# Optimization experiments

Measured on AMD Instinct MI355X. Metric: run time of the kernel, lower is better.

Reference implementation:

```python
import jax, jax.numpy as jnp
import numpy as np

TOP_K = 2
SMOOTHING = 0.9


def setup_inputs() -> dict:
    key = jax.random.key(0)
    k1, k2, k3 = jax.random.split(key, 3)
    T, D, E = 16384, 2048, 64
    x = jax.random.normal(k1, (T, D), dtype=jnp.float32)
    gate_w = jax.random.normal(k2, (D, E), dtype=jnp.float32) * (1.0 / np.sqrt(D))
    expert_loads = jax.random.uniform(k3, (E,), dtype=jnp.float32)
    expert_loads = expert_loads / jnp.sum(expert_loads)  # normalized load estimate
    return {"x": x, "gate_w": gate_w, "expert_loads": expert_loads}


def reference(x, gate_w, expert_loads):
    T, _ = x.shape
    E = gate_w.shape[1]
    # Gate projection: [T, D] @ [D, E] -> [T, E]
    logits = jnp.matmul(x, gate_w)
    # Load-balancing bias injection (ExpertLoadBalancer.get_balancing_biases):
    # bias = -(load - 1/E) * 2, added to logits for expert *selection* only.
    biases = -(expert_loads - 1.0 / E) * 2.0
    _, top_idx = jax.lax.top_k(logits + biases[None, :], TOP_K)  # [T, K] int32
    # Routing weights: softmax over the selected (unbiased) logits.
    top_logits = jnp.take_along_axis(logits, top_idx, axis=1)  # [T, K]
    routing_weights = jax.nn.softmax(top_logits, axis=-1)  # [T, K]
    # Vectorized load update (replaces the Python double loop in update_loads):
    # scatter-add routing weights per expert, normalize by token count, EMA-smooth.
    current_loads = jax.ops.segment_sum(
        routing_weights.reshape(-1), top_idx.reshape(-1), num_segments=E
    ) / T
    new_loads = SMOOTHING * expert_loads + (1.0 - SMOOTHING) * current_loads
    return routing_weights, top_idx, new_loads
```

## Files before the change

kernel.cpp:

```cpp
#include <hip/hip_runtime.h>

#define TT 16384
#define DD 2048
#define EE 64

typedef __attribute__((ext_vector_type(8))) short bf16x8;
typedef __attribute__((ext_vector_type(8))) unsigned short ushort8;
typedef __attribute__((ext_vector_type(4))) float f32x4;

__device__ __forceinline__ unsigned short bf16_rne(float f) {
    unsigned u = __float_as_uint(f);
    return (unsigned short)((u + 0x7FFFu + ((u >> 16) & 1u)) >> 16);
}
__device__ __forceinline__ float bf16_f32(unsigned short h) {
    return __uint_as_float(((unsigned)h) << 16);
}
__device__ __forceinline__ unsigned cvt_pk(float lo, float hi) {
    unsigned r;
    asm("v_cvt_pk_bf16_f32 %0, %1, %2" : "=v"(r) : "v"(lo), "v"(hi));
    return r;
}
__device__ __forceinline__ bf16x8 pack4(unsigned a, unsigned b, unsigned c, unsigned d) {
    union { unsigned u[4]; bf16x8 v; } t;
    t.u[0] = a; t.u[1] = b; t.u[2] = c; t.u[3] = d;
    return t.v;
}
__device__ __forceinline__ void gload16(void* lds, const void* g) {
    __builtin_amdgcn_global_load_lds(
        (const __attribute__((address_space(1))) unsigned int*)g,
        (__attribute__((address_space(3))) unsigned int*)lds, 16, 0, 0);
}

__global__ __launch_bounds__(256)
void wconv(const float* __restrict__ wg, unsigned short* __restrict__ wpack) {
    const int t = (int)blockIdx.x * 256 + threadIdx.x;
    const int K0 = t >> 9, h = (t >> 8) & 1, m = (t >> 6) & 3, lane = t & 63;
    const int e = m * 16 + (lane & 15);
    const int ks = K0 * 32 + (lane >> 4) * 8;
    ushort8 v;
#pragma unroll
    for (int j = 0; j < 8; ++j) {
        const float f = wg[(size_t)(ks + j) * EE + e];
        const unsigned short hi = bf16_rne(f);
        v[j] = h ? bf16_rne(f - bf16_f32(hi)) : hi;
    }
    *(ushort8*)(wpack + ((size_t)(K0 * 8 + h * 4 + m) * 64 + lane) * 8) = v;
}

__global__ __launch_bounds__(512, 4)
void gate_fused(const float* __restrict__ x, const unsigned short* __restrict__ wpack,
                const float* __restrict__ loads, float* __restrict__ out,
                float* __restrict__ binpart) {
    __shared__ __align__(16) float arena[12288];
    __shared__ float bins[2][64];

    const int tid = threadIdx.x, lane = tid & 63, w = tid >> 6;
    const int tg = w >> 2, q = w & 3;
    const int tb = (int)blockIdx.x;

    f32x4 acc[4] = {{0,0,0,0},{0,0,0,0},{0,0,0,0},{0,0,0,0}};

    auto stage_x = [&](int s, float* rb) {
#pragma unroll
        for (int i = 0; i < 2; ++i) {
            const int rowp = lane >> 3;
            const int r = i * 8 + rowp;
            const int c = (lane & 7) ^ rowp;
            gload16(rb + i * 256,
                    x + (size_t)(tb * 32 + tg * 16 + r) * DD + q * 512 + s * 32 + c * 4);
        }
    };
    auto loadW = [&](int t, bf16x8 (&wh)[4], bf16x8 (&wl)[4]) {
        const unsigned short* base = wpack + (size_t)(q * 16 + t) * 4096 + lane * 8;
#pragma unroll
        for (int m = 0; m < 4; ++m) {
            wh[m] = *(const bf16x8*)(base + (size_t)m * 512);
            wl[m] = *(const bf16x8*)(base + (size_t)(4 + m) * 512);
        }
    };
    auto compute = [&](const float* rb, bf16x8 (&wh)[4], bf16x8 (&wl)[4]) {
        const int r = lane & 15;
        const int kgc = (lane >> 4) << 1;
        const int sw = r & 7;
        const f32x4 va = *(const f32x4*)(rb + r * 32 + ((kgc) ^ sw) * 4);
        const f32x4 vb = *(const f32x4*)(rb + r * 32 + ((kgc + 1) ^ sw) * 4);
        const float cf[8] = {va.x, va.y, va.z, va.w, vb.x, vb.y, vb.z, vb.w};
        unsigned ph[4], pl[4];
#pragma unroll
        for (int j = 0; j < 4; ++j) {
            ph[j] = cvt_pk(cf[2 * j], cf[2 * j + 1]);
            const float h0 = __uint_as_float(ph[j] << 16);
            const float h1 = __uint_as_float(ph[j] & 0xFFFF0000u);
            pl[j] = cvt_pk(cf[2 * j] - h0, cf[2 * j + 1] - h1);
        }
        const bf16x8 bhi = pack4(ph[0], ph[1], ph[2], ph[3]);
        const bf16x8 blo = pack4(pl[0], pl[1], pl[2], pl[3]);
#pragma unroll
        for (int m = 0; m < 4; ++m) {
            acc[m] = __builtin_amdgcn_mfma_f32_16x16x32_bf16(wh[m], bhi, acc[m], 0, 0, 0);
            acc[m] = __builtin_amdgcn_mfma_f32_16x16x32_bf16(wh[m], blo, acc[m], 0, 0, 0);
            acc[m] = __builtin_amdgcn_mfma_f32_16x16x32_bf16(wl[m], bhi, acc[m], 0, 0, 0);
        }
    };

    float* ring = arena + (size_t)w * 1536;
    float *p0 = ring, *p1 = ring + 512, *p2 = ring + 1024;
    bf16x8 whA[4], wlA[4], whB[4], wlB[4];

    stage_x(0, p0);
    stage_x(1, p1);
    loadW(0, whA, wlA);
    asm volatile("s_waitcnt vmcnt(10)" ::: "memory");

#pragma unroll 1
    for (int s = 0; s < 14; s += 2) {
        stage_x(s + 2, p2);
        loadW(s + 1, whB, wlB);
        compute(p0, whA, wlA);
        asm volatile("s_waitcnt vmcnt(10)" ::: "memory");
        { float* t_ = p0; p0 = p1; p1 = p2; p2 = t_; }

        stage_x(s + 3, p2);
        loadW(s + 2, whA, wlA);
        compute(p0, whB, wlB);
        asm volatile("s_waitcnt vmcnt(10)" ::: "memory");
        { float* t_ = p0; p0 = p1; p1 = p2; p2 = t_; }
    }
    loadW(15, whB, wlB);
    compute(p0, whA, wlA);
    asm volatile("s_waitcnt vmcnt(8)" ::: "memory");
    compute(p1, whB, wlB);

    __syncthreads();
    float* accb = arena;
    if (q != 0) {
#pragma unroll
        for (int m = 0; m < 4; ++m)
            *(f32x4*)(accb + ((size_t)((q - 1) * 128 + tg * 64 + lane) * 20 + m * 4)) = acc[m];
    }
    __syncthreads();
    if (q != 0) return;

    f32x4 r[4];
#pragma unroll
    for (int m = 0; m < 4; ++m) {
        f32x4 s_ = acc[m];
#pragma unroll
        for (int qq = 0; qq < 3; ++qq) {
            const f32x4 t_ =
                *(const f32x4*)(accb + ((size_t)(qq * 128 + tg * 64 + lane) * 20 + m * 4));
            s_.x += t_.x; s_.y += t_.y; s_.z += t_.z; s_.w += t_.w;
        }
        r[m] = s_;
    }

    const int col = lane & 15;
    const int tok = tb * 32 + tg * 16 + col;
    const int erow = (lane >> 4) * 4;
    float v1 = -3.4e38f, u1 = 0.0f, v2 = -3.4e38f, u2 = 0.0f;
    int i1 = 0x7fffffff, i2 = 0x7fffffff;
#pragma unroll
    for (int m = 0; m < 4; ++m)
#pragma unroll
        for (int rr = 0; rr < 4; ++rr) {
            const int e = m * 16 + erow + rr;
            const float u = r[m][rr];
            const float b = u - (loads[e] - 0.015625f) * 2.0f;
            if ((b > v1) || (b == v1 && e < i1)) {
                v2 = v1; u2 = u1; i2 = i1;
                v1 = b;  u1 = u;  i1 = e;
            } else if ((b > v2) || (b == v2 && e < i2)) {
                v2 = b; u2 = u; i2 = e;
            }
        }
#pragma unroll
    for (int s = 0; s < 2; ++s) {
        const int mask = 16 << s;
        const float ov1 = __shfl_xor(v1, mask), ou1 = __shfl_xor(u1, mask);
        const float ov2 = __shfl_xor(v2, mask), ou2 = __shfl_xor(u2, mask);
        const int oi1 = __shfl_xor(i1, mask), oi2 = __shfl_xor(i2, mask);
        if ((ov1 > v1) || (ov1 == v1 && oi1 < i1)) {
            if ((v1 > ov2) || (v1 == ov2 && i1 < oi2)) { v2 = v1; u2 = u1; i2 = i1; }
            else                                        { v2 = ov2; u2 = ou2; i2 = oi2; }
            v1 = ov1; u1 = ou1; i1 = oi1;
        } else if ((ov1 > v2) || (ov1 == v2 && oi1 < i2)) {
            v2 = ov1; u2 = ou1; i2 = oi1;
        }
    }

    bins[tg][lane] = 0.0f;
    if (lane < 16) {
        const float mx = fmaxf(u1, u2);
        const float e1 = __expf(u1 - mx), e2 = __expf(u2 - mx);
        const float w1 = e1 / (e1 + e2), w2 = e2 / (e1 + e2);
        *(float2*)(out + 2 * tok) = make_float2(w1, w2);
        *(float2*)(out + 2 * TT + 2 * tok) = make_float2((float)i1, (float)i2);
        atomicAdd(&bins[tg][i1], w1);
        atomicAdd(&bins[tg][i2], w2);
    }
    binpart[(size_t)(tb * 2 + tg) * 64 + lane] = bins[tg][lane];
}

__global__ __launch_bounds__(1024)
void finalize(const float* __restrict__ binpart, const float* __restrict__ loads,
              float* __restrict__ out) {
    __shared__ float p[16][64];
    const int e = threadIdx.x & 63, sub = threadIdx.x >> 6;
    float s = 0.0f;
#pragma unroll
    for (int r = 0; r < 64; ++r)
        s += binpart[(size_t)(sub * 64 + r) * 64 + e];
    p[sub][e] = s;
    __syncthreads();
    if (sub == 0) {
        float tot = 0.0f;
#pragma unroll
        for (int k = 0; k < 16; ++k) tot += p[k][e];
        out[4 * TT + e] = 0.9f * loads[e] + 0.1f * (tot * (1.0f / 16384.0f));
    }
}

extern "C" void kernel_launch(void* const* d_in, const int* in_sizes, int n_in,
                              void* d_out, int out_size, void* d_ws, size_t ws_size,
                              hipStream_t stream) {
    const float* x = (const float*)d_in[0];
    const float* wg = (const float*)d_in[1];
    const float* loads = (const float*)d_in[2];
    float* out = (float*)d_out;

    unsigned short* wpack = (unsigned short*)d_ws;
    float* binpart = (float*)(wpack + (size_t)64 * 8 * 64 * 8);

    hipLaunchKernelGGL(wconv, dim3(128), dim3(256), 0, stream, wg, wpack);
    hipLaunchKernelGGL(gate_fused, dim3(512), dim3(512), 0, stream,
                       x, wpack, loads, out, binpart);
    hipLaunchKernelGGL(finalize, dim3(1), dim3(1024), 0, stream,
                       binpart, loads, out);
}
```

Measured before the change: 46.27 us.

## Halve gate block to 16 tokens and deepen weight prefetch with asm loads

Each gate block now has four waves covering 16 tokens instead of eight waves covering 32, and twice as many blocks are launched. Weight fragments are loaded through inline-asm global loads fenced by scheduling barriers, and are now prefetched one stage further ahead alongside the x tiles, with explicit vmcnt waits. The aim is better overlap of the x stream and weight loads with MFMA work, plus finer-grained scheduling. The cost is that every block still reads the whole packed weight matrix, so total L2 weight traffic doubles. The inline asm also takes control of instruction ordering away from the compiler.

After: 45.17 us. -2.4%, faster.

```diff
diff --git a/kernel.cpp b/kernel.cpp
--- a/kernel.cpp
+++ b/kernel.cpp
@@ -30,6 +30,11 @@
         (const __attribute__((address_space(1))) unsigned int*)g,
         (__attribute__((address_space(3))) unsigned int*)lds, 16, 0, 0);
 }
+__device__ __forceinline__ void ld16(bf16x8& d, const void* p) {
+    asm volatile("global_load_dwordx4 %0, %1, off"
+                 : "=&v"(d) : "v"(p) : "memory");
+}
+#define SB0() __builtin_amdgcn_sched_barrier(0)
 
 __global__ __launch_bounds__(256)
 void wconv(const float* __restrict__ wg, unsigned short* __restrict__ wpack) {
@@ -47,15 +52,14 @@
     *(ushort8*)(wpack + ((size_t)(K0 * 8 + h * 4 + m) * 64 + lane) * 8) = v;
 }
 
-__global__ __launch_bounds__(512, 4)
+__global__ __launch_bounds__(256, 4)
 void gate_fused(const float* __restrict__ x, const unsigned short* __restrict__ wpack,
                 const float* __restrict__ loads, float* __restrict__ out,
                 float* __restrict__ binpart) {
-    __shared__ __align__(16) float arena[12288];
-    __shared__ float bins[2][64];
-
-    const int tid = threadIdx.x, lane = tid & 63, w = tid >> 6;
-    const int tg = w >> 2, q = w & 3;
+    __shared__ __align__(16) float arena[6144];
+    __shared__ float bins[64];
+
+    const int tid = threadIdx.x, lane = tid & 63, q = tid >> 6;
     const int tb = (int)blockIdx.x;
 
     f32x4 acc[4] = {{0,0,0,0},{0,0,0,0},{0,0,0,0},{0,0,0,0}};
@@ -67,16 +71,15 @@
             const int r = i * 8 + rowp;
             const int c = (lane & 7) ^ rowp;
             gload16(rb + i * 256,
-                    x + (size_t)(tb * 32 + tg * 16 + r) * DD + q * 512 + s * 32 + c * 4);
+                    x + (size_t)(tb * 16 + r) * DD + q * 512 + s * 32 + c * 4);
         }
     };
-    auto loadW = [&](int t, bf16x8 (&wh)[4], bf16x8 (&wl)[4]) {
+    auto asmW = [&](int t, bf16x8 (&wh)[4], bf16x8 (&wl)[4]) {
         const unsigned short* base = wpack + (size_t)(q * 16 + t) * 4096 + lane * 8;
 #pragma unroll
-        for (int m = 0; m < 4; ++m) {
-            wh[m] = *(const bf16x8*)(base + (size_t)m * 512);
-            wl[m] = *(const bf16x8*)(base + (size_t)(4 + m) * 512);
-        }
+        for (int m = 0; m < 4; ++m) ld16(wh[m], base + (size_t)m * 512);
+#pragma unroll
+        for (int m = 0; m < 4; ++m) ld16(wl[m], base + (size_t)(4 + m) * 512);
     };
     auto compute = [&](const float* rb, bf16x8 (&wh)[4], bf16x8 (&wl)[4]) {
         const int r = lane & 15;
@@ -103,40 +106,58 @@
         }
     };
 
-    float* ring = arena + (size_t)w * 1536;
+    float* ring = arena + (size_t)q * 1536;
     float *p0 = ring, *p1 = ring + 512, *p2 = ring + 1024;
     bf16x8 whA[4], wlA[4], whB[4], wlB[4];
 
-    stage_x(0, p0);
-    stage_x(1, p1);
-    loadW(0, whA, wlA);
+    stage_x(0, p0); SB0();
+    asmW(0, whA, wlA); SB0();
+    stage_x(1, p1); SB0();
+    asmW(1, whB, wlB); SB0();
+    stage_x(2, p2); SB0();
+    asm volatile("s_waitcnt vmcnt(12)" ::: "memory");
+    SB0();
+    compute(p0, whA, wlA);
+    { float* t_ = p0; p0 = p1; p1 = p2; p2 = t_; }
+
+#pragma unroll 1
+    for (int s = 0; s < 12; s += 2) {
+        asmW(s + 2, whA, wlA); SB0();
+        stage_x(s + 3, p2); SB0();
+        asm volatile("s_waitcnt vmcnt(12)" ::: "memory");
+        SB0();
+        compute(p0, whB, wlB);
+        { float* t_ = p0; p0 = p1; p1 = p2; p2 = t_; }
+
+        asmW(s + 3, whB, wlB); SB0();
+        stage_x(s + 4, p2); SB0();
+        asm volatile("s_waitcnt vmcnt(12)" ::: "memory");
+        SB0();
+        compute(p0, whA, wlA);
+        { float* t_ = p0; p0 = p1; p1 = p2; p2 = t_; }
+    }
+    asmW(14, whA, wlA); SB0();
+    stage_x(15, p2); SB0();
+    asm volatile("s_waitcnt vmcnt(12)" ::: "memory");
+    SB0();
+    compute(p0, whB, wlB);
+    { float* t_ = p0; p0 = p1; p1 = p2; p2 = t_; }
+
+    asmW(15, whB, wlB); SB0();
     asm volatile("s_waitcnt vmcnt(10)" ::: "memory");
-
-#pragma unroll 1
-    for (int s = 0; s < 14; s += 2) {
-        stage_x(s + 2, p2);
-        loadW(s + 1, whB, wlB);
-        compute(p0, whA, wlA);
-        asm volatile("s_waitcnt vmcnt(10)" ::: "memory");
-        { float* t_ = p0; p0 = p1; p1 = p2; p2 = t_; }
-
-        stage_x(s + 3, p2);
-        loadW(s + 2, whA, wlA);
-        compute(p0, whB, wlB);
-        asm volatile("s_waitcnt vmcnt(10)" ::: "memory");
-        { float* t_ = p0; p0 = p1; p1 = p2; p2 = t_; }
-    }
-    loadW(15, whB, wlB);
+    SB0();
     compute(p0, whA, wlA);
-    asm volatile("s_waitcnt vmcnt(8)" ::: "memory");
-    compute(p1, whB, wlB);
+    { float* t_ = p0; p0 = p1; p1 = p2; p2 = t_; }
+    asm volatile("s_waitcnt vmcnt(0)" ::: "memory");
+    SB0();
+    compute(p0, whB, wlB);
 
     __syncthreads();
     float* accb = arena;
     if (q != 0) {
 #pragma unroll
         for (int m = 0; m < 4; ++m)
-            *(f32x4*)(accb + ((size_t)((q - 1) * 128 + tg * 64 + lane) * 20 + m * 4)) = acc[m];
+            *(f32x4*)(accb + ((size_t)((q - 1) * 64 + lane) * 20 + m * 4)) = acc[m];
     }
     __syncthreads();
     if (q != 0) return;
@@ -148,14 +169,14 @@
 #pragma unroll
         for (int qq = 0; qq < 3; ++qq) {
             const f32x4 t_ =
-                *(const f32x4*)(accb + ((size_t)(qq * 128 + tg * 64 + lane) * 20 + m * 4));
+                *(const f32x4*)(accb + ((size_t)(qq * 64 + lane) * 20 + m * 4));
             s_.x += t_.x; s_.y += t_.y; s_.z += t_.z; s_.w += t_.w;
         }
         r[m] = s_;
     }
 
     const int col = lane & 15;
-    const int tok = tb * 32 + tg * 16 + col;
+    const int tok = tb * 16 + col;
     const int erow = (lane >> 4) * 4;
     float v1 = -3.4e38f, u1 = 0.0f, v2 = -3.4e38f, u2 = 0.0f;
     int i1 = 0x7fffffff, i2 = 0x7fffffff;
@@ -188,17 +209,17 @@
         }
     }
 
-    bins[tg][lane] = 0.0f;
+    bins[lane] = 0.0f;
     if (lane < 16) {
         const float mx = fmaxf(u1, u2);
         const float e1 = __expf(u1 - mx), e2 = __expf(u2 - mx);
         const float w1 = e1 / (e1 + e2), w2 = e2 / (e1 + e2);
         *(float2*)(out + 2 * tok) = make_float2(w1, w2);
         *(float2*)(out + 2 * TT + 2 * tok) = make_float2((float)i1, (float)i2);
-        atomicAdd(&bins[tg][i1], w1);
-        atomicAdd(&bins[tg][i2], w2);
-    }
-    binpart[(size_t)(tb * 2 + tg) * 64 + lane] = bins[tg][lane];
+        atomicAdd(&bins[i1], w1);
+        atomicAdd(&bins[i2], w2);
+    }
+    binpart[(size_t)tb * 64 + lane] = bins[lane];
 }
 
 __global__ __launch_bounds__(1024)
@@ -232,7 +253,7 @@
     float* binpart = (float*)(wpack + (size_t)64 * 8 * 64 * 8);
 
     hipLaunchKernelGGL(wconv, dim3(128), dim3(256), 0, stream, wg, wpack);
-    hipLaunchKernelGGL(gate_fused, dim3(512), dim3(512), 0, stream,
+    hipLaunchKernelGGL(gate_fused, dim3(1024), dim3(256), 0, stream,
                        x, wpack, loads, out, binpart);
     hipLaunchKernelGGL(finalize, dim3(1), dim3(1024), 0, stream,
                        binpart, loads, out);
```

## Let each wave compute 32 tokens so weight fragments are reused twice

Applied to the files above, without the earlier changes.

The block shrinks from 512 to 256 threads. Each wave now handles 32 tokens using two accumulator sets, so each weight fragment loaded from global memory feeds two token tiles and weight traffic per token is halved. The K loop is fully unrolled into a three-stage ring for both x and W, with explicit waitcnt and sched_barrier placement, and top-k runs twice per wave. The cost is higher register pressure from triple-buffered weights and doubled accumulators, and fewer waves per block, which may reduce latency hiding.

Result: faster. 40.19 us (median of 3 runs) (-13.1%).

```diff
diff --git a/kernel.cpp b/kernel.cpp
--- a/kernel.cpp
+++ b/kernel.cpp
@@ -30,6 +30,7 @@
         (const __attribute__((address_space(1))) unsigned int*)g,
         (__attribute__((address_space(3))) unsigned int*)lds, 16, 0, 0);
 }
+#define SB0() __builtin_amdgcn_sched_barrier(0)
 
 __global__ __launch_bounds__(256)
 void wconv(const float* __restrict__ wg, unsigned short* __restrict__ wpack) {
@@ -47,43 +48,50 @@
     *(ushort8*)(wpack + ((size_t)(K0 * 8 + h * 4 + m) * 64 + lane) * 8) = v;
 }
 
-__global__ __launch_bounds__(512, 4)
+__global__ __launch_bounds__(256, 2)
 void gate_fused(const float* __restrict__ x, const unsigned short* __restrict__ wpack,
                 const float* __restrict__ loads, float* __restrict__ out,
                 float* __restrict__ binpart) {
     __shared__ __align__(16) float arena[12288];
-    __shared__ float bins[2][64];
-
-    const int tid = threadIdx.x, lane = tid & 63, w = tid >> 6;
-    const int tg = w >> 2, q = w & 3;
+    __shared__ float bins[64];
+
+    const int tid = threadIdx.x, lane = tid & 63, q = tid >> 6;
     const int tb = (int)blockIdx.x;
 
-    f32x4 acc[4] = {{0,0,0,0},{0,0,0,0},{0,0,0,0},{0,0,0,0}};
-
-    auto stage_x = [&](int s, float* rb) {
-#pragma unroll
-        for (int i = 0; i < 2; ++i) {
+    f32x4 a0[4] = {{0,0,0,0},{0,0,0,0},{0,0,0,0},{0,0,0,0}};
+    f32x4 a1[4] = {{0,0,0,0},{0,0,0,0},{0,0,0,0},{0,0,0,0}};
+
+    float* ring = arena + (size_t)q * 3072;
+    float *sp0 = ring, *sp1 = ring + 1024, *sp2 = ring + 2048;
+
+    auto stage_x = [&](int s, float* sb) {
+#pragma unroll
+        for (int i = 0; i < 4; ++i) {
             const int rowp = lane >> 3;
-            const int r = i * 8 + rowp;
             const int c = (lane & 7) ^ rowp;
-            gload16(rb + i * 256,
-                    x + (size_t)(tb * 32 + tg * 16 + r) * DD + q * 512 + s * 32 + c * 4);
-        }
-    };
-    auto loadW = [&](int t, bf16x8 (&wh)[4], bf16x8 (&wl)[4]) {
-        const unsigned short* base = wpack + (size_t)(q * 16 + t) * 4096 + lane * 8;
+            gload16(sb + i * 256,
+                    x + (size_t)(tb * 32 + i * 8 + rowp) * DD + q * 512 + s * 32 + c * 4);
+        }
+    };
+    auto loadW = [&](int s, bf16x8 (&wh)[4], bf16x8 (&wl)[4]) {
+        const unsigned short* base = wpack + (size_t)(q * 16 + s) * 4096 + lane * 8;
 #pragma unroll
         for (int m = 0; m < 4; ++m) {
             wh[m] = *(const bf16x8*)(base + (size_t)m * 512);
             wl[m] = *(const bf16x8*)(base + (size_t)(4 + m) * 512);
         }
     };
-    auto compute = [&](const float* rb, bf16x8 (&wh)[4], bf16x8 (&wl)[4]) {
-        const int r = lane & 15;
+    auto readx = [&](const float* sb, f32x4& va0, f32x4& vb0, f32x4& va1, f32x4& vb1) {
+        const int rl = lane & 15;
         const int kgc = (lane >> 4) << 1;
-        const int sw = r & 7;
-        const f32x4 va = *(const f32x4*)(rb + r * 32 + ((kgc) ^ sw) * 4);
-        const f32x4 vb = *(const f32x4*)(rb + r * 32 + ((kgc + 1) ^ sw) * 4);
+        const int sw = rl & 7;
+        va0 = *(const f32x4*)(sb + rl * 32 + ((kgc) ^ sw) * 4);
+        vb0 = *(const f32x4*)(sb + rl * 32 + ((kgc + 1) ^ sw) * 4);
+        va1 = *(const f32x4*)(sb + (16 + rl) * 32 + ((kgc) ^ sw) * 4);
+        vb1 = *(const f32x4*)(sb + (16 + rl) * 32 + ((kgc + 1) ^ sw) * 4);
+    };
+    auto domfma = [&](const f32x4& va, const f32x4& vb,
+                      bf16x8 (&wh)[4], bf16x8 (&wl)[4], f32x4 (&ac)[4]) {
         const float cf[8] = {va.x, va.y, va.z, va.w, vb.x, vb.y, vb.z, vb.w};
         unsigned ph[4], pl[4];
 #pragma unroll
@@ -97,108 +105,119 @@
         const bf16x8 blo = pack4(pl[0], pl[1], pl[2], pl[3]);
 #pragma unroll
         for (int m = 0; m < 4; ++m) {
-            acc[m] = __builtin_amdgcn_mfma_f32_16x16x32_bf16(wh[m], bhi, acc[m], 0, 0, 0);
-            acc[m] = __builtin_amdgcn_mfma_f32_16x16x32_bf16(wh[m], blo, acc[m], 0, 0, 0);
-            acc[m] = __builtin_amdgcn_mfma_f32_16x16x32_bf16(wl[m], bhi, acc[m], 0, 0, 0);
-        }
-    };
-
-    float* ring = arena + (size_t)w * 1536;
-    float *p0 = ring, *p1 = ring + 512, *p2 = ring + 1024;
-    bf16x8 whA[4], wlA[4], whB[4], wlB[4];
-
-    stage_x(0, p0);
-    stage_x(1, p1);
-    loadW(0, whA, wlA);
-    asm volatile("s_waitcnt vmcnt(10)" ::: "memory");
-
-#pragma unroll 1
-    for (int s = 0; s < 14; s += 2) {
-        stage_x(s + 2, p2);
-        loadW(s + 1, whB, wlB);
-        compute(p0, whA, wlA);
-        asm volatile("s_waitcnt vmcnt(10)" ::: "memory");
-        { float* t_ = p0; p0 = p1; p1 = p2; p2 = t_; }
-
-        stage_x(s + 3, p2);
-        loadW(s + 2, whA, wlA);
-        compute(p0, whB, wlB);
-        asm volatile("s_waitcnt vmcnt(10)" ::: "memory");
-        { float* t_ = p0; p0 = p1; p1 = p2; p2 = t_; }
-    }
-    loadW(15, whB, wlB);
-    compute(p0, whA, wlA);
-    asm volatile("s_waitcnt vmcnt(8)" ::: "memory");
-    compute(p1, whB, wlB);
+            ac[m] = __builtin_amdgcn_mfma_f32_16x16x32_bf16(wh[m], bhi, ac[m], 0, 0, 0);
+            ac[m] = __builtin_amdgcn_mfma_f32_16x16x32_bf16(wh[m], blo, ac[m], 0, 0, 0);
+            ac[m] = __builtin_amdgcn_mfma_f32_16x16x32_bf16(wl[m], bhi, ac[m], 0, 0, 0);
+        }
+    };
+
+    bf16x8 WH0[4], WO0[4], WH1[4], WO1[4], WH2[4], WO2[4];
+
+    stage_x(0, sp0); SB0();
+    loadW(0, WH0, WO0); SB0();
+    stage_x(1, sp1); SB0();
+    loadW(1, WH1, WO1); SB0();
+    stage_x(2, sp2); SB0();
+
+#define ITER(s, nsl, nwl, VM, DOW, DOS)                                   \
+    do {                                                                  \
+        asm volatile("s_waitcnt vmcnt(" #VM ")" ::: "memory"); SB0();     \
+        f32x4 va0, vb0, va1, vb1;                                         \
+        readx(sp##nsl, va0, vb0, va1, vb1); SB0();                        \
+        asm volatile("s_waitcnt lgkmcnt(0)" ::: "memory"); SB0();         \
+        if (DOW) loadW((s) + 2, WH##nwl, WO##nwl);                        \
+        SB0();                                                            \
+        if (DOS) stage_x((s) + 3, sp##nsl);                               \
+        SB0();                                                            \
+        domfma(va0, vb0, WH##nsl, WO##nsl, a0);                           \
+        domfma(va1, vb1, WH##nsl, WO##nsl, a1);                           \
+    } while (0)
+
+    ITER(0, 0, 2, 16, 1, 1);  ITER(1, 1, 0, 16, 1, 1);
+    ITER(2, 2, 1, 16, 1, 1);  ITER(3, 0, 2, 16, 1, 1);
+    ITER(4, 1, 0, 16, 1, 1);  ITER(5, 2, 1, 16, 1, 1);
+    ITER(6, 0, 2, 16, 1, 1);  ITER(7, 1, 0, 16, 1, 1);
+    ITER(8, 2, 1, 16, 1, 1);  ITER(9, 0, 2, 16, 1, 1);
+    ITER(10, 1, 0, 16, 1, 1); ITER(11, 2, 1, 16, 1, 1);
+    ITER(12, 0, 2, 16, 1, 1);
+    ITER(13, 1, 0, 16, 1, 0);
+    ITER(14, 2, 0, 12, 0, 0);
+    ITER(15, 0, 0, 0, 0, 0);
+#undef ITER
 
     __syncthreads();
-    float* accb = arena;
     if (q != 0) {
-#pragma unroll
-        for (int m = 0; m < 4; ++m)
-            *(f32x4*)(accb + ((size_t)((q - 1) * 128 + tg * 64 + lane) * 20 + m * 4)) = acc[m];
+        float* p = arena + (size_t)(q - 1) * 2304 + lane * 36;
+#pragma unroll
+        for (int m = 0; m < 4; ++m) {
+            *(f32x4*)(p + m * 4) = a0[m];
+            *(f32x4*)(p + 16 + m * 4) = a1[m];
+        }
     }
     __syncthreads();
     if (q != 0) return;
 
-    f32x4 r[4];
-#pragma unroll
-    for (int m = 0; m < 4; ++m) {
-        f32x4 s_ = acc[m];
-#pragma unroll
-        for (int qq = 0; qq < 3; ++qq) {
-            const f32x4 t_ =
-                *(const f32x4*)(accb + ((size_t)(qq * 128 + tg * 64 + lane) * 20 + m * 4));
-            s_.x += t_.x; s_.y += t_.y; s_.z += t_.z; s_.w += t_.w;
-        }
-        r[m] = s_;
-    }
-
+#pragma unroll 1
+    for (int qq = 0; qq < 3; ++qq) {
+        const float* p = arena + (size_t)qq * 2304 + lane * 36;
+#pragma unroll
+        for (int m = 0; m < 4; ++m) {
+            const f32x4 t0 = *(const f32x4*)(p + m * 4);
+            const f32x4 t1 = *(const f32x4*)(p + 16 + m * 4);
+            a0[m].x += t0.x; a0[m].y += t0.y; a0[m].z += t0.z; a0[m].w += t0.w;
+            a1[m].x += t1.x; a1[m].y += t1.y; a1[m].z += t1.z; a1[m].w += t1.w;
+        }
+    }
+
+    bins[lane] = 0.0f;
     const int col = lane & 15;
-    const int tok = tb * 32 + tg * 16 + col;
     const int erow = (lane >> 4) * 4;
-    float v1 = -3.4e38f, u1 = 0.0f, v2 = -3.4e38f, u2 = 0.0f;
-    int i1 = 0x7fffffff, i2 = 0x7fffffff;
-#pragma unroll
-    for (int m = 0; m < 4; ++m)
-#pragma unroll
-        for (int rr = 0; rr < 4; ++rr) {
-            const int e = m * 16 + erow + rr;
-            const float u = r[m][rr];
-            const float b = u - (loads[e] - 0.015625f) * 2.0f;
-            if ((b > v1) || (b == v1 && e < i1)) {
-                v2 = v1; u2 = u1; i2 = i1;
-                v1 = b;  u1 = u;  i1 = e;
-            } else if ((b > v2) || (b == v2 && e < i2)) {
-                v2 = b; u2 = u; i2 = e;
+    auto topk = [&](f32x4 (&r)[4], int tokbase) {
+        float v1 = -3.4e38f, u1 = 0.0f, v2 = -3.4e38f, u2 = 0.0f;
+        int i1 = 0x7fffffff, i2 = 0x7fffffff;
+#pragma unroll
+        for (int m = 0; m < 4; ++m)
+#pragma unroll
+            for (int rr = 0; rr < 4; ++rr) {
+                const int e = m * 16 + erow + rr;
+                const float u = r[m][rr];
+                const float b = u - (loads[e] - 0.015625f) * 2.0f;
+                if ((b > v1) || (b == v1 && e < i1)) {
+                    v2 = v1; u2 = u1; i2 = i1;
+                    v1 = b;  u1 = u;  i1 = e;
+                } else if ((b > v2) || (b == v2 && e < i2)) {
+                    v2 = b; u2 = u; i2 = e;
+                }
             }
-        }
-#pragma unroll
-    for (int s = 0; s < 2; ++s) {
-        const int mask = 16 << s;
-        const float ov1 = __shfl_xor(v1, mask), ou1 = __shfl_xor(u1, mask);
-        const float ov2 = __shfl_xor(v2, mask), ou2 = __shfl_xor(u2, mask);
-        const int oi1 = __shfl_xor(i1, mask), oi2 = __shfl_xor(i2, mask);
-        if ((ov1 > v1) || (ov1 == v1 && oi1 < i1)) {
-            if ((v1 > ov2) || (v1 == ov2 && i1 < oi2)) { v2 = v1; u2 = u1; i2 = i1; }
-            else                                        { v2 = ov2; u2 = ou2; i2 = oi2; }
-            v1 = ov1; u1 = ou1; i1 = oi1;
-        } else if ((ov1 > v2) || (ov1 == v2 && oi1 < i2)) {
-            v2 = ov1; u2 = ou1; i2 = oi1;
-        }
-    }
-
-    bins[tg][lane] = 0.0f;
-    if (lane < 16) {
-        const float mx = fmaxf(u1, u2);
-        const float e1 = __expf(u1 - mx), e2 = __expf(u2 - mx);
-        const float w1 = e1 / (e1 + e2), w2 = e2 / (e1 + e2);
-        *(float2*)(out + 2 * tok) = make_float2(w1, w2);
-        *(float2*)(out + 2 * TT + 2 * tok) = make_float2((float)i1, (float)i2);
-        atomicAdd(&bins[tg][i1], w1);
-        atomicAdd(&bins[tg][i2], w2);
-    }
-    binpart[(size_t)(tb * 2 + tg) * 64 + lane] = bins[tg][lane];
+#pragma unroll
+        for (int s = 0; s < 2; ++s) {
+            const int mask = 16 << s;
+            const float ov1 = __shfl_xor(v1, mask), ou1 = __shfl_xor(u1, mask);
+            const float ov2 = __shfl_xor(v2, mask), ou2 = __shfl_xor(u2, mask);
+            const int oi1 = __shfl_xor(i1, mask), oi2 = __shfl_xor(i2, mask);
+            if ((ov1 > v1) || (ov1 == v1 && oi1 < i1)) {
+                if ((v1 > ov2) || (v1 == ov2 && i1 < oi2)) { v2 = v1; u2 = u1; i2 = i1; }
+                else                                        { v2 = ov2; u2 = ou2; i2 = oi2; }
+                v1 = ov1; u1 = ou1; i1 = oi1;
+            } else if ((ov1 > v2) || (ov1 == v2 && oi1 < i2)) {
+                v2 = ov1; u2 = ou1; i2 = oi1;
+            }
+        }
+        if (lane < 16) {
+            const int tok = tokbase + col;
+            const float mx = fmaxf(u1, u2);
+            const float e1 = __expf(u1 - mx), e2 = __expf(u2 - mx);
+            const float w1 = e1 / (e1 + e2), w2 = e2 / (e1 + e2);
+            *(float2*)(out + 2 * tok) = make_float2(w1, w2);
+            *(float2*)(out + 2 * TT + 2 * tok) = make_float2((float)i1, (float)i2);
+            atomicAdd(&bins[i1], w1);
+            atomicAdd(&bins[i2], w2);
+        }
+    };
+    topk(a0, tb * 32);
+    topk(a1, tb * 32 + 16);
+
+    binpart[(size_t)tb * 64 + lane] = bins[lane];
 }
 
 __global__ __launch_bounds__(1024)
@@ -208,8 +227,8 @@
     const int e = threadIdx.x & 63, sub = threadIdx.x >> 6;
     float s = 0.0f;
 #pragma unroll
-    for (int r = 0; r < 64; ++r)
-        s += binpart[(size_t)(sub * 64 + r) * 64 + e];
+    for (int r = 0; r < 32; ++r)
+        s += binpart[(size_t)(sub * 32 + r) * 64 + e];
     p[sub][e] = s;
     __syncthreads();
     if (sub == 0) {
@@ -232,7 +251,7 @@
     float* binpart = (float*)(wpack + (size_t)64 * 8 * 64 * 8);
 
     hipLaunchKernelGGL(wconv, dim3(128), dim3(256), 0, stream, wg, wpack);
-    hipLaunchKernelGGL(gate_fused, dim3(512), dim3(512), 0, stream,
+    hipLaunchKernelGGL(gate_fused, dim3(512), dim3(256), 0, stream,
                        x, wpack, loads, out, binpart);
     hipLaunchKernelGGL(finalize, dim3(1), dim3(1024), 0, stream,
                        binpart, loads, out);
```
